# Optimization experiments

Measured on AMD Instinct MI355X. Metric: run time of the kernel, lower is better.

## Reference

```python
import jax, jax.numpy as jnp
import numpy as np

H = 8            # heads
M = 256          # num_landmarks
PINV_ITERS = 6
PAD = 16         # residual_conv_kernel(33)//2


def layernorm(x, g, b, eps=1e-5):
    mu = x.mean(-1, keepdims=True)
    var = ((x - mu) ** 2).mean(-1, keepdims=True)
    return (x - mu) * jax.lax.rsqrt(var + eps) * g + b


def moore_penrose_pinv(x, iters=PINV_ITERS):
    # iterative Moore-Penrose pseudo-inverse (Nystromformer)
    abs_x = jnp.abs(x)
    col = abs_x.sum(-1)
    row = abs_x.sum(-2)
    z = jnp.swapaxes(x, -1, -2) / (jnp.max(col) * jnp.max(row))
    eye = jnp.eye(x.shape[-1], dtype=x.dtype)
    for _ in range(iters):
        xz = x @ z
        z = 0.25 * z @ (13.0 * eye - xz @ (15.0 * eye - xz @ (7.0 * eye - xz)))
    return z


def attn_block(y, ln1_g, ln1_b, w_qkv, w_out, b_out, res_w,
               ln2_g, ln2_b, w1, b1, w2, b2):
    B, N, D = y.shape
    inner = w_qkv.shape[1] // 3
    dh = inner // H
    xn = layernorm(y, ln1_g, ln1_b)
    qkv = xn @ w_qkv                      # [B,N,3*inner]
    q, k, v = jnp.split(qkv, 3, axis=-1)
    to_heads = lambda t: t.reshape(B, N, H, dh).transpose(0, 2, 1, 3)  # [B,H,N,dh]
    q, k, v = map(to_heads, (q, k, v))
    q = q * (dh ** -0.5)
    l = N // M                            # tokens per landmark (N % M == 0 here)
    q_l = q.reshape(B, H, M, l, dh).mean(3)  # sum/l == mean -> [B,H,M,dh]
    k_l = k.reshape(B, H, M, l, dh).mean(3)
    attn1 = jax.nn.softmax(jnp.einsum('bhnd,bhmd->bhnm', q, k_l), axis=-1)
    attn2 = jax.nn.softmax(jnp.einsum('bhid,bhjd->bhij', q_l, k_l), axis=-1)
    attn3 = jax.nn.softmax(jnp.einsum('bhmd,bhnd->bhmn', q_l, k), axis=-1)
    attn2_inv = moore_penrose_pinv(attn2)
    out = (attn1 @ attn2_inv) @ (attn3 @ v)   # [B,H,N,dh]
    # depthwise residual conv over sequence dim: v as NCHW with C=H, Hdim=N, Wdim=dh
    res = jax.lax.conv_general_dilated(
        v, res_w, window_strides=(1, 1), padding=[(PAD, PAD), (0, 0)],
        dimension_numbers=('NCHW', 'OIHW', 'NCHW'), feature_group_count=H)
    out = out + res
    out = out.transpose(0, 2, 1, 3).reshape(B, N, inner)
    y = y + out @ w_out + b_out
    yn = layernorm(y, ln2_g, ln2_b)
    hdn = jax.nn.gelu(yn @ w1 + b1, approximate=False)
    return y + hdn @ w2 + b2


def setup_inputs() -> dict:
    key = jax.random.key(0)
    ks = jax.random.split(key, 8)
    B, N, D, NB = 4, 4096, 256, 2
    inner = D
    p = lambda k, shp: jax.random.normal(k, shp, jnp.float32) * 0.02
    return {
        'x': jax.random.normal(ks[0], (B, N, D), jnp.float32),
        'ln1_g': jnp.ones((NB, D), jnp.float32),
        'ln1_b': jnp.zeros((NB, D), jnp.float32),
        'w_qkv': p(ks[1], (NB, D, 3 * inner)),
        'w_out': p(ks[2], (NB, inner, D)),
        'b_out': jnp.zeros((NB, D), jnp.float32),
        'res_w': p(ks[3], (NB, H, 1, 33, 1)),
        'ln2_g': jnp.ones((NB, D), jnp.float32),
        'ln2_b': jnp.zeros((NB, D), jnp.float32),
        'w1': p(ks[4], (NB, D, 2 * D)),
        'b1': jnp.zeros((NB, 2 * D), jnp.float32),
        'w2': p(ks[5], (NB, 2 * D, D)),
        'b2': jnp.zeros((NB, D), jnp.float32),
    }


def reference(x, ln1_g, ln1_b, w_qkv, w_out, b_out, res_w,
              ln2_g, ln2_b, w1, b1, w2, b2):
    y = x
    for i in range(ln1_g.shape[0]):
        y = attn_block(y, ln1_g[i], ln1_b[i], w_qkv[i], w_out[i], b_out[i],
                       res_w[i], ln2_g[i], ln2_b[i], w1[i], b1[i], w2[i], b2[i])
    return y
```

## Files before the change

kernel.cpp:

```cpp
#include <hip/hip_runtime.h>
#include <math.h>

typedef float f32x4 __attribute__((ext_vector_type(4)));
typedef short s16x8 __attribute__((ext_vector_type(8)));
typedef unsigned short u16;
typedef unsigned int u32;

#define MFMA16(a,b,c) __builtin_amdgcn_mfma_f32_16x16x32_bf16((a),(b),(c),0,0,0)
#define AS1 __attribute__((address_space(1)))
#define AS3 __attribute__((address_space(3)))

__device__ __forceinline__ void dma16(const u16* g, u16* l){
  __builtin_amdgcn_global_load_lds((const AS1 u32*)g, (AS3 u32*)l, 16, 0, 0);
}

__device__ __forceinline__ float bf2f(u16 u){
  union { unsigned int i; float f; } v; v.i = ((unsigned int)u)<<16; return v.f;
}
__device__ __forceinline__ u16 f2bf(float f){
  union { float f; unsigned int i; } v; v.f = f;
  unsigned int x = v.i;
  return (u16)((x + 0x7fffu + ((x>>16)&1u))>>16);
}

enum { EPI_QKV=0, EPI_BIAS_GELU=3 };

template<int EPI>
__global__ __launch_bounds__(256)
void kgemm2(const u16* __restrict__ A, const u16* __restrict__ BT, int K, int lda, int ldb,
            const float* __restrict__ bias, u16* __restrict__ outb, int ldc,
            u16* __restrict__ qo, u16* __restrict__ ko, u16* __restrict__ vo,
            u16* __restrict__ qlm, u16* __restrict__ klm)
{
  __shared__ __align__(16) u16 As[128*32];
  __shared__ __align__(16) u16 Bs[128*32];
  const int tid = threadIdx.x;
  const int w = tid>>6, wy = w>>1, wx = w&1, l = tid&63, q = l>>4, ln = l&15;
  const int m0 = blockIdx.x*128, n0 = blockIdx.y*128;
  const int lrow = l>>2, lch = l&3;

  f32x4 acc[4][4];
  #pragma unroll
  for (int i=0;i<4;i++)
    #pragma unroll
    for (int j=0;j<4;j++){ acc[i][j][0]=0.f; acc[i][j][1]=0.f; acc[i][j][2]=0.f; acc[i][j][3]=0.f; }

  for (int k0=0; k0<K; k0+=32){
    #pragma unroll
    for (int c=0;c<2;c++){
      int row = 32*w + 16*c + lrow;
      int gch = lch ^ ((row>>1)&3);
      dma16(A + (long)(m0+row)*lda + k0 + gch*8, &As[(32*w+16*c)*32]);
      dma16(BT + (long)(n0+row)*ldb + k0 + gch*8, &Bs[(32*w+16*c)*32]);
    }
    __syncthreads();
    s16x8 af[4], bfr[4];
    #pragma unroll
    for (int mt=0;mt<4;mt++){
      int row = wy*64 + mt*16 + ln;
      af[mt] = *(const s16x8*)&As[row*32 + ((q ^ ((row>>1)&3))<<3)];
    }
    #pragma unroll
    for (int nt=0;nt<4;nt++){
      int row = wx*64 + nt*16 + ln;
      bfr[nt] = *(const s16x8*)&Bs[row*32 + ((q ^ ((row>>1)&3))<<3)];
    }
    #pragma unroll
    for (int mt=0;mt<4;mt++)
      #pragma unroll
      for (int nt=0;nt<4;nt++)
        acc[mt][nt] = MFMA16(af[mt], bfr[nt], acc[mt][nt]);
    __syncthreads();
  }

  #pragma unroll
  for (int mt=0;mt<4;mt++)
  #pragma unroll
  for (int nt=0;nt<4;nt++){
    int ncol = n0 + wx*64 + nt*16 + ln;
    if (EPI==EPI_QKV){
      int sel = ncol>>8, hd = ncol&255, h = hd>>5, d = hd&31;
      u16* dst = sel==0 ? qo : (sel==1 ? ko : vo);
      float sc2 = (sel==0) ? 0.17677669529663689f : 1.f;
      float s = 0.f;
      #pragma unroll
      for (int r=0;r<4;r++){
        int mrow = m0 + wy*64 + mt*16 + q*4 + r;
        int b = mrow>>12, n = mrow&4095;
        float v = acc[mt][nt][r]*sc2;
        dst[(((long)(b*8+h)*4096 + n)<<5) + d] = f2bf(v);
        s += v;
      }
      if (sel < 2){
        s += __shfl_xor(s, 16);
        s += __shfl_xor(s, 32);
        if (q == 0){
          int mrow0 = m0 + wy*64 + mt*16;
          int b = mrow0>>12, grp = (mrow0&4095)>>4;
          u16* ldst = (sel==0) ? qlm : klm;
          ldst[(((long)(b*8+h)*256 + grp)<<5) + d] = f2bf(s*(1.0f/16.0f));
        }
      }
    } else {
      #pragma unroll
      for (int r=0;r<4;r++){
        int mrow = m0 + wy*64 + mt*16 + q*4 + r;
        float x = acc[mt][nt][r] + bias[ncol];
        float g = 0.5f*x*(1.0f + erff(x*0.70710678118654752f));
        outb[(long)mrow*ldc + ncol] = f2bf(g);
      }
    }
  }
}

__global__ __launch_bounds__(256)
void kgemmLN(const u16* __restrict__ A, const u16* __restrict__ BT, int K,
             const float* __restrict__ bias, const float* __restrict__ base,
             float* __restrict__ yout,
             const float* __restrict__ lng, const float* __restrict__ lnb,
             u16* __restrict__ xnout)
{
  __shared__ __align__(16) u16 As[64*32];
  __shared__ __align__(16) u16 Bs[256*32];
  __shared__ float red[64][4];
  const int tid = threadIdx.x;
  const int w = tid>>6, l = tid&63, q = l>>4, ln = l&15;
  const int m0 = blockIdx.x*64;

  f32x4 acc[4][4];
  #pragma unroll
  for (int i=0;i<4;i++)
    #pragma unroll
    for (int j=0;j<4;j++){ acc[i][j][0]=0.f; acc[i][j][1]=0.f; acc[i][j][2]=0.f; acc[i][j][3]=0.f; }

  for (int k0=0; k0<K; k0+=32){
    {
      int row = w*16 + (l>>2);
      int gch = (l&3) ^ ((row>>1)&3);
      dma16(A + (long)(m0+row)*K + k0 + gch*8, &As[(w*16)*32]);
    }
    #pragma unroll
    for (int c=0;c<4;c++){
      int row = c*64 + w*16 + (l>>2);
      int gch = (l&3) ^ ((row>>1)&3);
      dma16(BT + (long)row*K + k0 + gch*8, &Bs[(c*64+w*16)*32]);
    }
    __syncthreads();
    s16x8 af[4], bfr[4];
    #pragma unroll
    for (int mt=0;mt<4;mt++){
      int row = mt*16 + ln;
      af[mt] = *(const s16x8*)&As[row*32 + ((q ^ ((row>>1)&3))<<3)];
    }
    #pragma unroll
    for (int nt=0;nt<4;nt++){
      int row = w*64 + nt*16 + ln;
      bfr[nt] = *(const s16x8*)&Bs[row*32 + ((q ^ ((row>>1)&3))<<3)];
    }
    #pragma unroll
    for (int mt=0;mt<4;mt++)
      #pragma unroll
      for (int nt=0;nt<4;nt++)
        acc[mt][nt] = MFMA16(af[mt], bfr[nt], acc[mt][nt]);
    __syncthreads();
  }

  float rb[4];
  #pragma unroll
  for (int nt=0;nt<4;nt++) rb[nt] = bias[w*64 + nt*16 + ln];
  #pragma unroll
  for (int mt=0;mt<4;mt++)
  #pragma unroll
  for (int r=0;r<4;r++){
    long rowb = (long)(m0 + mt*16 + q*4 + r)*256;
    #pragma unroll
    for (int nt=0;nt<4;nt++){
      int col = w*64 + nt*16 + ln;
      float v = base[rowb + col] + acc[mt][nt][r] + rb[nt];
      acc[mt][nt][r] = v;
      yout[rowb + col] = v;
    }
  }
  #pragma unroll
  for (int mt=0;mt<4;mt++)
  #pragma unroll
  for (int r=0;r<4;r++){
    float s = acc[mt][0][r]+acc[mt][1][r]+acc[mt][2][r]+acc[mt][3][r];
    s += __shfl_xor(s,1); s += __shfl_xor(s,2); s += __shfl_xor(s,4); s += __shfl_xor(s,8);
    if (ln==0) red[mt*16+q*4+r][w] = s;
  }
  __syncthreads();
  float mu[4][4];
  #pragma unroll
  for (int mt=0;mt<4;mt++)
  #pragma unroll
  for (int r=0;r<4;r++){
    int row = mt*16+q*4+r;
    mu[mt][r] = (red[row][0]+red[row][1]+red[row][2]+red[row][3])*(1.0f/256.0f);
  }
  __syncthreads();
  #pragma unroll
  for (int mt=0;mt<4;mt++)
  #pragma unroll
  for (int r=0;r<4;r++){
    float vs = 0.f;
    #pragma unroll
    for (int nt=0;nt<4;nt++){ float d = acc[mt][nt][r]-mu[mt][r]; vs += d*d; }
    vs += __shfl_xor(vs,1); vs += __shfl_xor(vs,2); vs += __shfl_xor(vs,4); vs += __shfl_xor(vs,8);
    if (ln==0) red[mt*16+q*4+r][w] = vs;
  }
  __syncthreads();
  float rg[4], rbb[4];
  #pragma unroll
  for (int nt=0;nt<4;nt++){ int col = w*64+nt*16+ln; rg[nt]=lng[col]; rbb[nt]=lnb[col]; }
  #pragma unroll
  for (int mt=0;mt<4;mt++)
  #pragma unroll
  for (int r=0;r<4;r++){
    int row = mt*16+q*4+r;
    float rs = rsqrtf((red[row][0]+red[row][1]+red[row][2]+red[row][3])*(1.0f/256.0f) + 1e-5f);
    long rowb = (long)(m0 + row)*256;
    #pragma unroll
    for (int nt=0;nt<4;nt++){
      int col = w*64 + nt*16 + ln;
      float d = acc[mt][nt][r]-mu[mt][r];
      xnout[rowb + col] = f2bf(d*rs*rg[nt] + rbb[nt]);
    }
  }
}

__device__ __forceinline__ int swidx(int row, int col){
  int cc = col>>3;
  int sl = (cc&24)|((cc&7)^((row>>1)&7));
  return row*256 + sl*8 + (col&7);
}
__device__ __forceinline__ int slot8(int ca, int row){
  return ((ca&24)|((ca&7)^((row>>1)&7)))<<3;
}

__device__ __forceinline__ void stage256(const u16* __restrict__ g, u16* lds, int w, int l){
  const int drow = l>>5, dch = l&31;
  #pragma unroll
  for (int c=0;c<16;c++){
    int base = (c*8 + w)*2;
    int row = base + drow;
    int gch = (dch&24) | ((dch&7) ^ ((row>>1)&7));
    dma16(g + (long)row*256 + gch*8, &lds[base*256]);
  }
}
__device__ __forceinline__ void stage32(const u16* __restrict__ g, u16* lds, int w, int l){
  const int drow = l>>5, dch = l&31;
  #pragma unroll
  for (int c=0;c<2;c++){
    int base = (c*8 + w)*2;
    int row = base + drow;
    int gch = (dch&24) | ((dch&7) ^ ((row>>1)&7));
    dma16(g + (long)row*256 + gch*8, &lds[base*256]);
  }
}
__device__ __forceinline__ void stage16(const u16* __restrict__ g, u16* lds, int w, int l){
  const int drow = l>>5, dch = l&31;
  int row = w*2 + drow;
  int gch = (dch&24) | ((dch&7) ^ ((row>>1)&7));
  dma16(g + (long)row*256 + gch*8, &lds[(w*2)*256]);
}

__device__ __forceinline__ void loadBf(const u16* bL, int w, int l, s16x8 (&bw)[2][8]){
  const int q=l>>4, ln=l&15, wn0=w*32;
  #pragma unroll
  for (int nt=0;nt<2;nt++)
    #pragma unroll
    for (int kq=0;kq<8;kq++){
      int n = wn0 + nt*16 + ln, ca = kq*4+q;
      bw[nt][kq] = *(const s16x8*)&bL[n*256 + slot8(ca, n)];
    }
}

__device__ __forceinline__ void multAr(const u16* aL, int arow0, const s16x8 (&bw)[2][8],
                                       int l, f32x4 (&acc)[2][2]){
  const int q=l>>4, ln=l&15;
  #pragma unroll
  for (int mt=0;mt<2;mt++)
    #pragma unroll
    for (int nt=0;nt<2;nt++){ acc[mt][nt][0]=0.f; acc[mt][nt][1]=0.f; acc[mt][nt][2]=0.f; acc[mt][nt][3]=0.f; }
  #pragma unroll
  for (int kq=0;kq<8;kq++){
    int ca = kq*4+q;
    s16x8 af[2];
    #pragma unroll
    for (int mt=0;mt<2;mt++){
      int r = arow0 + mt*16 + ln;
      af[mt] = *(const s16x8*)&aL[r*256 + slot8(ca, r)];
    }
    #pragma unroll
    for (int mt=0;mt<2;mt++)
      #pragma unroll
      for (int nt=0;nt<2;nt++)
        acc[mt][nt] = MFMA16(af[mt], bw[nt][kq], acc[mt][nt]);
  }
}

__device__ __forceinline__ void multHr(const u16* hL, const s16x8 (&bw)[2][8],
                                       int l, f32x4 (&hacc)[2]){
  const int q=l>>4, ln=l&15;
  hacc[0][0]=0.f; hacc[0][1]=0.f; hacc[0][2]=0.f; hacc[0][3]=0.f;
  hacc[1][0]=0.f; hacc[1][1]=0.f; hacc[1][2]=0.f; hacc[1][3]=0.f;
  #pragma unroll
  for (int kq=0;kq<8;kq++){
    int ca = kq*4+q;
    s16x8 af = *(const s16x8*)&hL[ln*256 + slot8(ca, ln)];
    hacc[0] = MFMA16(af, bw[0][kq], hacc[0]);
    hacc[1] = MFMA16(af, bw[1][kq], hacc[1]);
  }
}

__device__ __forceinline__ void polyinit13(const u16* aL, int arow0, int w, int l, f32x4 (&poly)[2][2]){
  const int q=l>>4, ln=l&15, wn0=w*32;
  #pragma unroll
  for (int mt=0;mt<2;mt++)
  #pragma unroll
  for (int nt=0;nt<2;nt++)
  #pragma unroll
  for (int r=0;r<4;r++){
    int row = arow0 + mt*16 + q*4 + r;
    int col = wn0 + nt*16 + ln;
    poly[mt][nt][r] = 13.f*bf2f(aL[swidx(row,col)]);
  }
}
__device__ __forceinline__ void init13H(const u16* hL, int w, int l, f32x4 (&hpoly)[2]){
  const int q=l>>4, ln=l&15, wn0=w*32;
  #pragma unroll
  for (int nt=0;nt<2;nt++)
  #pragma unroll
  for (int r=0;r<4;r++)
    hpoly[nt][r] = 13.f*bf2f(hL[swidx(q*4+r, wn0+nt*16+ln)]);
}
__device__ __forceinline__ void polyaxpy(f32x4 (&poly)[2][2], const f32x4 (&acc)[2][2], float sc){
  #pragma unroll
  for (int mt=0;mt<2;mt++)
    #pragma unroll
    for (int nt=0;nt<2;nt++)
      #pragma unroll
      for (int r=0;r<4;r++) poly[mt][nt][r] += sc*acc[mt][nt][r];
}
__device__ __forceinline__ void axpyH(f32x4 (&hpoly)[2], const f32x4 (&hacc)[2], float sc){
  #pragma unroll
  for (int nt=0;nt<2;nt++)
    #pragma unroll
    for (int r=0;r<4;r++) hpoly[nt][r] += sc*hacc[nt][r];
}
__device__ __forceinline__ void writeT(u16* Ts, const f32x4 (&acc)[2][2], int w, int l, float sc){
  const int q=l>>4, ln=l&15, wn0=w*32;
  #pragma unroll
  for (int mt=0;mt<2;mt++)
  #pragma unroll
  for (int nt=0;nt<2;nt++)
  #pragma unroll
  for (int r=0;r<4;r++){
    int row = mt*16 + q*4 + r;
    int col = wn0 + nt*16 + ln;
    Ts[swidx(row,col)] = f2bf(sc*acc[mt][nt][r]);
  }
}
__device__ __forceinline__ void writeH(u16* Hs, const f32x4 (&hacc)[2], int w, int l){
  const int q=l>>4, ln=l&15, wn0=w*32;
  #pragma unroll
  for (int nt=0;nt<2;nt++)
  #pragma unroll
  for (int r=0;r<4;r++)
    Hs[swidx(q*4+r, wn0+nt*16+ln)] = f2bf(hacc[nt][r]);
}
__device__ __forceinline__ void epi_poly(u16* __restrict__ out, int rowbase,
                                         const f32x4 (&poly)[2][2], int w, int l, float sc){
  const int q=l>>4, ln=l&15, wn0=w*32;
  #pragma unroll
  for (int mt=0;mt<2;mt++)
  #pragma unroll
  for (int nt=0;nt<2;nt++)
  #pragma unroll
  for (int r=0;r<4;r++){
    int row = rowbase + mt*16 + q*4 + r;
    int col = wn0 + nt*16 + ln;
    out[(long)row*256 + col] = f2bf(sc*poly[mt][nt][r]);
  }
}
__device__ __forceinline__ void epiH(u16* __restrict__ out, const f32x4 (&hpoly)[2],
                                     int w, int l, float sc){
  const int q=l>>4, ln=l&15, wn0=w*32;
  #pragma unroll
  for (int nt=0;nt<2;nt++)
  #pragma unroll
  for (int r=0;r<4;r++)
    out[(long)(q*4+r)*256 + wn0+nt*16+ln] = f2bf(sc*hpoly[nt][r]);
}

__device__ __forceinline__ void mult32(const u16* aL, int arow0, const u16* bL,
                                       int w, int l, f32x4 (&acc)[2][2]){
  const int q=l>>4, ln=l&15, wn0=w*32;
  #pragma unroll
  for (int mt=0;mt<2;mt++)
    #pragma unroll
    for (int nt=0;nt<2;nt++){ acc[mt][nt][0]=0.f; acc[mt][nt][1]=0.f; acc[mt][nt][2]=0.f; acc[mt][nt][3]=0.f; }
  #pragma unroll
  for (int kq=0;kq<8;kq++){
    int ca = kq*4+q;
    s16x8 af[2];
    #pragma unroll
    for (int mt=0;mt<2;mt++){
      int r = arow0 + mt*16 + ln;
      af[mt] = *(const s16x8*)&aL[r*256 + slot8(ca,r)];
    }
    #pragma unroll
    for (int nt=0;nt<2;nt++){
      int n = wn0 + nt*16 + ln;
      s16x8 bfr = *(const s16x8*)&bL[n*256 + slot8(ca,n)];
      acc[0][nt] = MFMA16(af[0], bfr, acc[0][nt]);
      acc[1][nt] = MFMA16(af[1], bfr, acc[1][nt]);
    }
  }
}

__global__ __launch_bounds__(512)
void kw0(const float* __restrict__ cs_p, float* __restrict__ scal,
         const float* __restrict__ num_p, const float* __restrict__ den_p,
         const u16* __restrict__ X, u16* __restrict__ W0, u16* __restrict__ h0)
{
  __shared__ __align__(16) u16 Wf[65536];
  __shared__ __align__(16) u16 Ts[8192];
  const int tid=threadIdx.x, w=tid>>6, l=tid&63;
  const int bid=blockIdx.x, xcd=bid&7, j=bid>>3;
  const int batch = xcd*4 + (j>>3), slab = j&7;

  stage256(X + (long)batch*65536, Wf, w, l);

  float* red = (float*)Ts;
  float mx = 0.f;
  for (int i=tid;i<8192;i+=512){
    float s = 0.f;
    #pragma unroll
    for (int c=0;c<8;c++) s += cs_p[(long)c*8192 + i];
    mx = fmaxf(mx, s);
  }
  red[tid] = mx; __syncthreads();
  for (int s=256;s>0;s>>=1){ if (tid<s) red[tid] = fmaxf(red[tid], red[tid+s]); __syncthreads(); }
  float s0 = 1.0f/red[0];
  if (bid==0 && tid==0) scal[0] = s0;

  f32x4 acc[2][2];
  mult32(Wf, slab*32, Wf, w, l, acc);
  {
    const int q=l>>4, ln=l&15, wn0=w*32;
    u16* ob = W0 + (long)batch*65536;
    #pragma unroll
    for (int mt=0;mt<2;mt++)
    #pragma unroll
    for (int nt=0;nt<2;nt++)
    #pragma unroll
    for (int r=0;r<4;r++){
      int row = slab*32 + mt*16 + q*4 + r;
      int col = wn0 + nt*16 + ln;
      ob[(long)row*256 + col] = f2bf(acc[mt][nt][r]*s0);
    }
  }

  if (slab==0){
    __syncthreads();
    float (*lt)[257] = (float(*)[257])Wf;
    for (int i=tid;i<8192;i+=512){
      int m = i>>5, d = i&31;
      float sn = 0.f, sd = 0.f;
      #pragma unroll
      for (int c=0;c<8;c++){
        sn += num_p[((long)(c*32+batch))*8192 + i];
        sd += den_p[(c*32+batch)*256 + m];
      }
      lt[d][m] = sn/sd;
    }
    __syncthreads();
    u16* o = h0 + (long)batch*8192;
    for (int j2=tid;j2<8192;j2+=512){
      int d = j2>>8, m = j2&255;
      o[j2] = f2bf(lt[d][m]);
    }
  }
}

__global__ __launch_bounds__(512)
void kiter(const u16* __restrict__ Win, u16* __restrict__ Wout,
           const u16* __restrict__ hin, u16* __restrict__ hout)
{
  __shared__ __align__(16) u16 Wf[65536];
  __shared__ __align__(16) u16 Ts[8192];
  __shared__ __align__(16) u16 Hs[4096];
  const int tid=threadIdx.x, w=tid>>6, l=tid&63;
  const int bid=blockIdx.x, xcd=bid&7, j=bid>>3;
  const int batch = xcd*4 + (j>>3), slab = j&7;
  const bool hrole = (slab&3)==0;
  const int hr0 = (slab>>2)*16;

  stage256(Win + (long)batch*65536, Wf, w, l);
  if (hrole) stage16(hin + (long)batch*8192 + hr0*256, Hs, w, l);
  __syncthreads();

  s16x8 bw[2][8];
  loadBf(Wf, w, l, bw);

  f32x4 acc[2][2], poly[2][2];
  f32x4 hacc[2], hpoly[2];

  polyinit13(Wf, slab*32, w, l, poly);
  multAr(Wf, slab*32, bw, l, acc);
  polyaxpy(poly, acc, -15.f);
  if (hrole){
    init13H(Hs, w, l, hpoly);
    multHr(Hs, bw, l, hacc);
    axpyH(hpoly, hacc, -15.f);
  }
  __syncthreads();
  writeT(Ts, acc, w, l, 1.f);
  if (hrole) writeH(Hs, hacc, w, l);
  __syncthreads();
  multAr(Ts, 0, bw, l, acc);
  polyaxpy(poly, acc, 7.f);
  if (hrole){ multHr(Hs, bw, l, hacc); axpyH(hpoly, hacc, 7.f); }
  __syncthreads();
  writeT(Ts, acc, w, l, 1.f);
  if (hrole) writeH(Hs, hacc, w, l);
  __syncthreads();
  multAr(Ts, 0, bw, l, acc);
  polyaxpy(poly, acc, -1.f);
  epi_poly(Wout + (long)batch*65536, slab*32, poly, w, l, 0.25f);
  if (hrole){
    multHr(Hs, bw, l, hacc);
    axpyH(hpoly, hacc, -1.f);
    epiH(hout + (long)batch*8192 + hr0*256, hpoly, w, l, 0.25f);
  }
}

__global__ __launch_bounds__(512)
void ktail(const u16* __restrict__ W5, const u16* __restrict__ h5,
           const u16* __restrict__ XT, const float* __restrict__ scal,
           u16* __restrict__ uT)
{
  __shared__ __align__(16) u16 Wf[65536];
  __shared__ __align__(16) u16 Ts[8192];
  const int tid=threadIdx.x, w=tid>>6, l=tid&63;
  const int batch = blockIdx.x;

  stage256(W5 + (long)batch*65536, Wf, w, l);
  stage32(h5 + (long)batch*8192, Ts, w, l);
  __syncthreads();

  s16x8 bw[2][8];
  loadBf(Wf, w, l, bw);

  f32x4 acc[2][2], poly[2][2];
  polyinit13(Ts, 0, w, l, poly);
  multAr(Ts, 0, bw, l, acc);
  polyaxpy(poly, acc, -15.f);
  __syncthreads(); writeT(Ts, acc, w, l, 1.f); __syncthreads();
  multAr(Ts, 0, bw, l, acc);
  polyaxpy(poly, acc, 7.f);
  __syncthreads(); writeT(Ts, acc, w, l, 1.f); __syncthreads();
  multAr(Ts, 0, bw, l, acc);
  polyaxpy(poly, acc, -1.f);
  __syncthreads();
  writeT(Ts, poly, w, l, 0.25f);
  stage256(XT + (long)batch*65536, Wf, w, l);
  __syncthreads();
  loadBf(Wf, w, l, bw);
  multAr(Ts, 0, bw, l, acc);
  const float s0 = scal[0];
  {
    const int q=l>>4, ln=l&15, wn0=w*32;
    u16* ob = uT + (long)batch*8192;
    #pragma unroll
    for (int mt=0;mt<2;mt++)
    #pragma unroll
    for (int nt=0;nt<2;nt++)
    #pragma unroll
    for (int r=0;r<4;r++){
      int row = mt*16 + q*4 + r;
      int col = wn0 + nt*16 + ln;
      ob[(long)row*256 + col] = f2bf(acc[mt][nt][r]*s0);
    }
  }
}

__global__ __launch_bounds__(256)
void kattn23(const u16* __restrict__ ql, const u16* __restrict__ kl,
             u16* __restrict__ X, u16* __restrict__ XT, float* __restrict__ cs_p,
             const u16* __restrict__ kk, const u16* __restrict__ vv,
             float* __restrict__ num_p, float* __restrict__ den_p)
{
  __shared__ __align__(16) u16 Pbuf[4][64][40];
  __shared__ __align__(16) u16 vT[32][40];
  __shared__ float qrow[32][33];
  __shared__ float psum[32][4];
  __shared__ float rsum[32];
  int bh = blockIdx.y;
  int tid = threadIdx.x, w = tid>>6, l = tid&63, q = l>>4, ln = l&15;

  if (blockIdx.x < 8){
    int r0 = blockIdx.x*32;
    int c = tid;
    #pragma unroll
    for (int i=0;i<4;i++){
      int e = c*4+i; int rr = e>>5, dd = e&31;
      qrow[rr][dd] = bf2f(ql[((long)bh*256 + r0+rr)*32 + dd]);
    }
    float kc[32];
    {
      const u16* kp = kl + ((long)bh*256 + c)*32;
      #pragma unroll
      for (int d=0;d<32;d++) kc[d] = bf2f(kp[d]);
    }
    __syncthreads();
    float er[32]; float colacc = 0.f;
    for (int r=0;r<32;r++){
      float s = 0.f;
      #pragma unroll
      for (int d=0;d<32;d++) s += qrow[r][d]*kc[d];
      float e = __expf(s);
      er[r] = e;
      float wsum = e;
      #pragma unroll
      for (int m=1;m<64;m<<=1) wsum += __shfl_xor(wsum, m);
      if (l==0) psum[r][w] = wsum;
    }
    __syncthreads();
    if (c<32) rsum[c] = psum[c][0]+psum[c][1]+psum[c][2]+psum[c][3];
    __syncthreads();
    for (int r=0;r<32;r++){
      float x = er[r]/rsum[r];
      u16 xb = f2bf(x);
      X [((long)bh*256 + r0+r)*256 + c] = xb;
      XT[((long)bh*256 + c)*256 + r0+r] = xb;
      colacc += x;
    }
    cs_p[(long)blockIdx.x*8192 + bh*256 + c] = colacc;
    return;
  }

  int chunk = blockIdx.x - 8;
  f32x4 z4; z4[0]=0.f; z4[1]=0.f; z4[2]=0.f; z4[3]=0.f;
  f32x4 acc[4][2]; f32x4 dacc[4];
  #pragma unroll
  for (int mt=0;mt<4;mt++){ dacc[mt]=z4; acc[mt][0]=z4; acc[mt][1]=z4; }
  const u16* qlb = ql + (long)bh*8192;
  const u16* kb  = kk + (long)bh*131072;
  const u16* vb  = vv + (long)bh*131072;
  int vn = tid>>3, vd = (tid&7)*4;
  for (int s=0;s<16;s++){
    int n0 = chunk*512 + s*32;
    ushort4 vx = *(const ushort4*)(vb + (long)(n0+vn)*32 + vd);
    vT[vd+0][vn]=vx.x; vT[vd+1][vn]=vx.y; vT[vd+2][vn]=vx.z; vT[vd+3][vn]=vx.w;
    __syncthreads();
    s16x8 bk[2];
    #pragma unroll
    for (int nt=0;nt<2;nt++) bk[nt] = *(const s16x8*)(kb + (long)(n0 + nt*16 + ln)*32 + q*8);
    #pragma unroll
    for (int mt=0;mt<4;mt++){
      s16x8 aq = *(const s16x8*)(qlb + (long)(w*64 + mt*16 + ln)*32 + q*8);
      #pragma unroll
      for (int nt=0;nt<2;nt++){
        f32x4 sf = MFMA16(aq, bk[nt], z4);
        f32x4 ef;
        #pragma unroll
        for (int r=0;r<4;r++) ef[r] = __expf(sf[r]);
        dacc[mt] += ef;
        #pragma unroll
        for (int r=0;r<4;r++) Pbuf[w][mt*16 + q*4 + r][nt*16 + ln] = f2bf(ef[r]);
      }
    }
    #pragma unroll
    for (int mt=0;mt<4;mt++){
      s16x8 ap = *(const s16x8*)&Pbuf[w][mt*16 + ln][q*8];
      #pragma unroll
      for (int nt=0;nt<2;nt++){
        s16x8 bv = *(const s16x8*)&vT[nt*16 + ln][q*8];
        acc[mt][nt] = MFMA16(ap, bv, acc[mt][nt]);
      }
    }
    __syncthreads();
  }
  #pragma unroll
  for (int mt=0;mt<4;mt++)
    #pragma unroll
    for (int r=0;r<4;r++){
      float x = dacc[mt][r];
      x += __shfl_xor(x,1); x += __shfl_xor(x,2); x += __shfl_xor(x,4); x += __shfl_xor(x,8);
      dacc[mt][r] = x;
    }
  long pbase = (long)(chunk*32 + bh);
  #pragma unroll
  for (int mt=0;mt<4;mt++)
    #pragma unroll
    for (int nt=0;nt<2;nt++)
      #pragma unroll
      for (int r=0;r<4;r++){
        int mg = w*64 + mt*16 + q*4 + r;
        num_p[pbase*8192 + (long)mg*32 + nt*16 + ln] = acc[mt][nt][r];
      }
  if (ln==0){
    #pragma unroll
    for (int mt=0;mt<4;mt++)
      #pragma unroll
      for (int r=0;r<4;r++)
        den_p[pbase*256 + w*64 + mt*16 + q*4 + r] = dacc[mt][r];
  }
}

__global__ __launch_bounds__(256)
void kattn1u(const u16* __restrict__ qq, const u16* __restrict__ kl, const u16* __restrict__ uT,
             const u16* __restrict__ vv, const float* __restrict__ rw,
             u16* __restrict__ aoutb)
{
  int nch = blockIdx.x, bh = blockIdx.y;
  int b = bh>>3, h = bh&7;
  int tid = threadIdx.x, w = tid>>6, l = tid&63, q = l>>4, ln = l&15;
  __shared__ __align__(16) u16 Pbuf[4][32][40];
  __shared__ __align__(16) u16 vtile[160][36];
  int r0g = nch*128;
  const u16* vb = vv + (long)bh*131072;
  #pragma unroll
  for (int it=0; it<5; it++){
    int slot = tid + it*256;
    int rr = slot>>3, c = (slot&7)*4;
    int s = r0g - 16 + rr;
    ushort4 val; val.x=0; val.y=0; val.z=0; val.w=0;
    if (s>=0 && s<4096) val = *(const ushort4*)(vb + (long)s*32 + c);
    *(ushort4*)&vtile[rr][c] = val;
  }
  __syncthreads();

  f32x4 z4; z4[0]=0.f; z4[1]=0.f; z4[2]=0.f; z4[3]=0.f;
  f32x4 acc[2][2]; f32x4 dacc[2];
  #pragma unroll
  for (int mt=0;mt<2;mt++){ dacc[mt]=z4; acc[mt][0]=z4; acc[mt][1]=z4; }
  const u16* qb  = qq + (long)bh*131072;
  const u16* klb = kl + (long)bh*8192;
  const u16* ub  = uT + (long)bh*8192;
  int r0 = r0g + w*32;
  for (int s=0;s<8;s++){
    s16x8 bk[2];
    #pragma unroll
    for (int nt=0;nt<2;nt++) bk[nt] = *(const s16x8*)(klb + (long)(s*32 + nt*16 + ln)*32 + q*8);
    #pragma unroll
    for (int mt=0;mt<2;mt++){
      s16x8 aq = *(const s16x8*)(qb + (long)(r0 + mt*16 + ln)*32 + q*8);
      #pragma unroll
      for (int nt=0;nt<2;nt++){
        f32x4 sf = MFMA16(aq, bk[nt], z4);
        f32x4 ef;
        #pragma unroll
        for (int r=0;r<4;r++) ef[r] = __expf(sf[r]);
        dacc[mt] += ef;
        #pragma unroll
        for (int r=0;r<4;r++) Pbuf[w][mt*16 + q*4 + r][nt*16 + ln] = f2bf(ef[r]);
      }
    }
    #pragma unroll
    for (int mt=0;mt<2;mt++){
      s16x8 ap = *(const s16x8*)&Pbuf[w][mt*16 + ln][q*8];
      #pragma unroll
      for (int nt=0;nt<2;nt++){
        s16x8 bu = *(const s16x8*)(ub + (long)(nt*16 + ln)*256 + s*32 + q*8);
        acc[mt][nt] = MFMA16(ap, bu, acc[mt][nt]);
      }
    }
  }
  #pragma unroll
  for (int mt=0;mt<2;mt++)
    #pragma unroll
    for (int r=0;r<4;r++){
      float x = dacc[mt][r];
      x += __shfl_xor(x,1); x += __shfl_xor(x,2); x += __shfl_xor(x,4); x += __shfl_xor(x,8);
      dacc[mt][r] = x;
    }

  const float* wp = rw + h*33;
  float w_[33];
  #pragma unroll
  for (int j=0;j<33;j++) w_[j] = wp[j];

  #pragma unroll
  for (int mt=0;mt<2;mt++){
    int nl = w*32 + mt*16 + q*4;
    #pragma unroll
    for (int nt=0;nt<2;nt++){
      int d = nt*16 + ln;
      float vvv[36];
      #pragma unroll
      for (int j=0;j<36;j++) vvv[j] = bf2f(vtile[nl + j][d]);
      #pragma unroll
      for (int r=0;r<4;r++){
        float cv = 0.f;
        #pragma unroll
        for (int j=0;j<33;j++) cv += w_[j]*vvv[r+j];
        int n = r0 + mt*16 + q*4 + r;
        long oidx = ((long)b*4096 + n)*256 + h*32 + d;
        aoutb[oidx] = f2bf(acc[mt][nt][r]/dacc[mt][r] + cv);
      }
    }
  }
}

__global__ __launch_bounds__(256)
void kcvtln(const float* __restrict__ xin, const float* __restrict__ lg, const float* __restrict__ lb,
            u16* __restrict__ xn,
            const float* __restrict__ wqkv, const float* __restrict__ wout,
            const float* __restrict__ w1, const float* __restrict__ w2,
            u16* __restrict__ wqkvT, u16* __restrict__ woutT,
            u16* __restrict__ w1T, u16* __restrict__ w2T)
{
  __shared__ float t[32][33];
  int z = blockIdx.x;
  if (z < 4096){
    int w = threadIdx.x>>6, l = threadIdx.x&63;
    long row = (long)z*4 + w;
    float4 v = ((const float4*)(xin + row*256))[l];
    float s = v.x+v.y+v.z+v.w;
    #pragma unroll
    for (int m=1;m<64;m<<=1) s += __shfl_xor(s, m);
    float mu = s*(1.0f/256.0f);
    float dx=v.x-mu, dy=v.y-mu, dz=v.z-mu, dw=v.w-mu;
    float s2 = dx*dx+dy*dy+dz*dz+dw*dw;
    #pragma unroll
    for (int m=1;m<64;m<<=1) s2 += __shfl_xor(s2, m);
    float rs = rsqrtf(s2*(1.0f/256.0f) + 1e-5f);
    float4 gg = ((const float4*)lg)[l];
    float4 bb = ((const float4*)lb)[l];
    ushort4 o;
    o.x = f2bf(dx*rs*gg.x + bb.x);
    o.y = f2bf(dy*rs*gg.y + bb.y);
    o.z = f2bf(dz*rs*gg.z + bb.z);
    o.w = f2bf(dw*rs*gg.w + bb.w);
    *(ushort4*)(xn + row*256 + l*4) = o;
    return;
  }
  z -= 4096;
  const float* src; u16* dst; int K, Nn, bx, by;
  if (z < 384){      int i=z/192, r=z%192; src=wqkv+(long)i*196608; dst=wqkvT+(long)i*196608; K=256; Nn=768; bx=r%24; by=r/24; }
  else if (z < 512){ int zz=z-384; int i=zz/64, r=zz%64; src=wout+(long)i*65536; dst=woutT+(long)i*65536; K=256; Nn=256; bx=r%8; by=r/8; }
  else if (z < 768){ int zz=z-512; int i=zz/128, r=zz%128; src=w1+(long)i*131072; dst=w1T+(long)i*131072; K=256; Nn=512; bx=r%16; by=r/16; }
  else {             int zz=z-768; int i=zz/128, r=zz%128; src=w2+(long)i*131072; dst=w2T+(long)i*131072; K=512; Nn=256; bx=r%8; by=r/8; }
  int n0 = bx*32, k0 = by*32;
  int tx = threadIdx.x&31, ty = threadIdx.x>>5;
  #pragma unroll
  for (int i=0;i<4;i++) t[ty+i*8][tx] = src[(long)(k0+ty+i*8)*Nn + n0+tx];
  __syncthreads();
  #pragma unroll
  for (int i=0;i<4;i++) dst[(long)(n0+ty+i*8)*K + k0+tx] = f2bf(t[tx][ty+i*8]);
}

extern "C" void kernel_launch(void* const* d_in, const int* in_sizes, int n_in,
                              void* d_out, int out_size, void* d_ws, size_t ws_size,
                              hipStream_t stream)
{
  const float* x    = (const float*)d_in[0];
  const float* ln1g = (const float*)d_in[1];
  const float* ln1b = (const float*)d_in[2];
  const float* wqkv = (const float*)d_in[3];
  const float* wout = (const float*)d_in[4];
  const float* bout = (const float*)d_in[5];
  const float* resw = (const float*)d_in[6];
  const float* ln2g = (const float*)d_in[7];
  const float* ln2b = (const float*)d_in[8];
  const float* w1   = (const float*)d_in[9];
  const float* b1   = (const float*)d_in[10];
  const float* w2   = (const float*)d_in[11];
  const float* b2   = (const float*)d_in[12];
  float* y = (float*)d_out;
  char* ws = (char*)d_ws;

  u16* xn    = (u16*)(ws + 0);
  u16* qb    = (u16*)(ws + 8388608);
  u16* kb    = (u16*)(ws + 16777216);
  u16* vb    = (u16*)(ws + 25165824);
  u16* ql    = (u16*)(ws + 33554432);
  u16* kl    = (u16*)(ws + 34078720);
  u16* X     = (u16*)(ws + 34603008);
  u16* XT    = (u16*)(ws + 38797312);
  u16* h0b   = (u16*)(ws + 42991616);
  u16* WA    = (u16*)(ws + 51380224);
  u16* WB    = (u16*)(ws + 55574528);
  u16* hA    = (u16*)(ws + 68157440);
  u16* hB    = (u16*)(ws + 72351744);
  float* num_p = (float*)(ws + 76546048);
  float* den_p = (float*)(ws + 84934656);
  float* cs_p  = (float*)(ws + 85196800);
  float* scal  = (float*)(ws + 85458944);
  u16* uT    = (u16*)(ws + 85459200);
  u16* aoutb = (u16*)(ws + 85983488);
  u16* wqkvT = (u16*)(ws + 94372096);
  u16* woutT = (u16*)(ws + 95158528);
  u16* w1T   = (u16*)(ws + 95420672);
  u16* w2T   = (u16*)(ws + 95944960);
  u16* hdn   = (u16*)(ws + 51380224);

  (void)in_sizes; (void)n_in; (void)out_size; (void)ws_size;

  kcvtln<<<5120,256,0,stream>>>(x, ln1g, ln1b, xn,
      wqkv, wout, w1, w2, wqkvT, woutT, w1T, w2T);

  for (int i=0;i<2;i++){
    kgemm2<EPI_QKV><<<dim3(128,6),256,0,stream>>>(xn, wqkvT + (long)i*196608, 256, 256, 256,
        nullptr, nullptr, 0, qb,kb,vb, ql,kl);
    kattn23<<<dim3(16,32),256,0,stream>>>(ql, kl, X, XT, cs_p, kb, vb, num_p, den_p);

    kw0<<<256,512,0,stream>>>(cs_p, scal, num_p, den_p, X, WA, h0b);
    u16 *Wi = WA, *Wo = WB, *hi = h0b, *ho = hA;
    for (int it=0; it<5; it++){
      kiter<<<256,512,0,stream>>>(Wi, Wo, hi, ho);
      u16* t = Wi; Wi = Wo; Wo = t;
      hi = ho; ho = (ho == hA) ? hB : hA;
    }
    ktail<<<32,512,0,stream>>>(Wi, hi, XT, scal, uT);

    kattn1u<<<dim3(32,32),256,0,stream>>>(qb, kl, uT, vb, resw + i*264, aoutb);
    kgemmLN<<<256,256,0,stream>>>(aoutb, woutT + (long)i*65536, 256,
        bout + i*256, i==0 ? x : y, y, ln2g + i*256, ln2b + i*256, xn);
    kgemm2<EPI_BIAS_GELU><<<dim3(128,4),256,0,stream>>>(xn, w1T + (long)i*131072, 256, 256, 256,
        b1 + i*512, hdn, 512, nullptr,nullptr,nullptr, nullptr,nullptr);
    kgemmLN<<<256,256,0,stream>>>(hdn, w2T + (long)i*131072, 512,
        b2 + i*256, y, y, ln1g + 256, ln1b + 256, xn);
  }
}
```

Measured before the change: 501.6 us.

## Double-buffer V tile, hoist Q fragments, transpose conv V tile for vector reads

In kattn23, the V tile is now double-buffered in shared memory. The next tile is loaded from global memory while the current one is being consumed, which removes one barrier per iteration. Q-landmark fragments are hoisted out of the loop in both attention kernels. In kattn1u, the residual-conv V tile is stored transposed so each thread reads 36 consecutive values with 9 ushort4 loads instead of 36 scalar strided loads. These changes add shared memory and register pressure, and the transposed scalar LDS stores may cause bank conflicts.

After: 621.0 us. 23.8% more time.

```diff
diff --git a/kernel.cpp b/kernel.cpp
--- a/kernel.cpp
+++ b/kernel.cpp
@@ -594,7 +594,7 @@
              float* __restrict__ num_p, float* __restrict__ den_p)
 {
   __shared__ __align__(16) u16 Pbuf[4][64][40];
-  __shared__ __align__(16) u16 vT[32][40];
+  __shared__ __align__(16) u16 vT2[2][32][40];
   __shared__ float qrow[32][33];
   __shared__ float psum[32][4];
   __shared__ float rsum[32];
@@ -650,21 +650,28 @@
   const u16* qlb = ql + (long)bh*8192;
   const u16* kb  = kk + (long)bh*131072;
   const u16* vb  = vv + (long)bh*131072;
+  s16x8 aq[4];
+  #pragma unroll
+  for (int mt=0;mt<4;mt++) aq[mt] = *(const s16x8*)(qlb + (long)(w*64 + mt*16 + ln)*32 + q*8);
   int vn = tid>>3, vd = (tid&7)*4;
+  {
+    ushort4 vx = *(const ushort4*)(vb + (long)(chunk*512+vn)*32 + vd);
+    vT2[0][vd+0][vn]=vx.x; vT2[0][vd+1][vn]=vx.y; vT2[0][vd+2][vn]=vx.z; vT2[0][vd+3][vn]=vx.w;
+  }
+  __syncthreads();
   for (int s=0;s<16;s++){
+    int cur = s&1;
+    ushort4 vnx;
+    if (s<15) vnx = *(const ushort4*)(vb + (long)(chunk*512+(s+1)*32+vn)*32 + vd);
     int n0 = chunk*512 + s*32;
-    ushort4 vx = *(const ushort4*)(vb + (long)(n0+vn)*32 + vd);
-    vT[vd+0][vn]=vx.x; vT[vd+1][vn]=vx.y; vT[vd+2][vn]=vx.z; vT[vd+3][vn]=vx.w;
-    __syncthreads();
     s16x8 bk[2];
     #pragma unroll
     for (int nt=0;nt<2;nt++) bk[nt] = *(const s16x8*)(kb + (long)(n0 + nt*16 + ln)*32 + q*8);
     #pragma unroll
     for (int mt=0;mt<4;mt++){
-      s16x8 aq = *(const s16x8*)(qlb + (long)(w*64 + mt*16 + ln)*32 + q*8);
       #pragma unroll
       for (int nt=0;nt<2;nt++){
-        f32x4 sf = MFMA16(aq, bk[nt], z4);
+        f32x4 sf = MFMA16(aq[mt], bk[nt], z4);
         f32x4 ef;
         #pragma unroll
         for (int r=0;r<4;r++) ef[r] = __expf(sf[r]);
@@ -678,9 +685,13 @@
       s16x8 ap = *(const s16x8*)&Pbuf[w][mt*16 + ln][q*8];
       #pragma unroll
       for (int nt=0;nt<2;nt++){
-        s16x8 bv = *(const s16x8*)&vT[nt*16 + ln][q*8];
+        s16x8 bv = *(const s16x8*)&vT2[cur][nt*16 + ln][q*8];
         acc[mt][nt] = MFMA16(ap, bv, acc[mt][nt]);
       }
+    }
+    if (s<15){
+      int nxt = cur^1;
+      vT2[nxt][vd+0][vn]=vnx.x; vT2[nxt][vd+1][vn]=vnx.y; vT2[nxt][vd+2][vn]=vnx.z; vT2[nxt][vd+3][vn]=vnx.w;
     }
     __syncthreads();
   }
@@ -720,7 +731,7 @@
   int b = bh>>3, h = bh&7;
   int tid = threadIdx.x, w = tid>>6, l = tid&63, q = l>>4, ln = l&15;
   __shared__ __align__(16) u16 Pbuf[4][32][40];
-  __shared__ __align__(16) u16 vtile[160][36];
+  __shared__ __align__(16) u16 vtileT[32][164];
   int r0g = nch*128;
   const u16* vb = vv + (long)bh*131072;
   #pragma unroll
@@ -730,7 +741,7 @@
     int s = r0g - 16 + rr;
     ushort4 val; val.x=0; val.y=0; val.z=0; val.w=0;
     if (s>=0 && s<4096) val = *(const ushort4*)(vb + (long)s*32 + c);
-    *(ushort4*)&vtile[rr][c] = val;
+    vtileT[c+0][rr]=val.x; vtileT[c+1][rr]=val.y; vtileT[c+2][rr]=val.z; vtileT[c+3][rr]=val.w;
   }
   __syncthreads();
 
@@ -742,16 +753,18 @@
   const u16* klb = kl + (long)bh*8192;
   const u16* ub  = uT + (long)bh*8192;
   int r0 = r0g + w*32;
+  s16x8 aq[2];
+  #pragma unroll
+  for (int mt=0;mt<2;mt++) aq[mt] = *(const s16x8*)(qb + (long)(r0 + mt*16 + ln)*32 + q*8);
   for (int s=0;s<8;s++){
     s16x8 bk[2];
     #pragma unroll
     for (int nt=0;nt<2;nt++) bk[nt] = *(const s16x8*)(klb + (long)(s*32 + nt*16 + ln)*32 + q*8);
     #pragma unroll
     for (int mt=0;mt<2;mt++){
-      s16x8 aq = *(const s16x8*)(qb + (long)(r0 + mt*16 + ln)*32 + q*8);
       #pragma unroll
       for (int nt=0;nt<2;nt++){
-        f32x4 sf = MFMA16(aq, bk[nt], z4);
+        f32x4 sf = MFMA16(aq[mt], bk[nt], z4);
         f32x4 ef;
         #pragma unroll
         for (int r=0;r<4;r++) ef[r] = __expf(sf[r]);
@@ -791,8 +804,13 @@
     for (int nt=0;nt<2;nt++){
       int d = nt*16 + ln;
       float vvv[36];
-      #pragma unroll
-      for (int j=0;j<36;j++) vvv[j] = bf2f(vtile[nl + j][d]);
+      const u16* vp = &vtileT[d][nl];
+      #pragma unroll
+      for (int jj=0;jj<9;jj++){
+        ushort4 vq = *(const ushort4*)(vp + jj*4);
+        vvv[jj*4+0]=bf2f(vq.x); vvv[jj*4+1]=bf2f(vq.y);
+        vvv[jj*4+2]=bf2f(vq.z); vvv[jj*4+3]=bf2f(vq.w);
+      }
       #pragma unroll
       for (int r=0;r<4;r++){
         float cv = 0.f;
```

## Replace final pinv iteration with row-slab polynomial chain in split tail kernel

Applied to the files above, without the earlier changes.

Drops one full 256x256 Newton-Schulz iteration launch. In its place the new tail kernel applies the remaining polynomial steps only to the 32-row h slab, blending them through a fixed linear combination (gpoly) before multiplying by XT. The tail work is split over two blocks per batch, and the XT staging is overlapped with the polynomial chain. This removes a large matrix-matrix pass in exchange for a long serial chain of small row-slab products with many barriers, and its numerical equivalence to the original iteration is not obvious.

Result: no change. 493.3 us (-1.7%).

```diff
diff --git a/kernel.cpp b/kernel.cpp
--- a/kernel.cpp
+++ b/kernel.cpp
@@ -248,16 +248,6 @@
     dma16(g + (long)row*256 + gch*8, &lds[base*256]);
   }
 }
-__device__ __forceinline__ void stage32(const u16* __restrict__ g, u16* lds, int w, int l){
-  const int drow = l>>5, dch = l&31;
-  #pragma unroll
-  for (int c=0;c<2;c++){
-    int base = (c*8 + w)*2;
-    int row = base + drow;
-    int gch = (dch&24) | ((dch&7) ^ ((row>>1)&7));
-    dma16(g + (long)row*256 + gch*8, &lds[base*256]);
-  }
-}
 __device__ __forceinline__ void stage16(const u16* __restrict__ g, u16* lds, int w, int l){
   const int drow = l>>5, dch = l&31;
   int row = w*2 + drow;
@@ -349,6 +339,10 @@
     #pragma unroll
     for (int r=0;r<4;r++) hpoly[nt][r] += sc*hacc[nt][r];
 }
+__device__ __forceinline__ void zeroH(f32x4 (&p)[2]){
+  p[0][0]=0.f; p[0][1]=0.f; p[0][2]=0.f; p[0][3]=0.f;
+  p[1][0]=0.f; p[1][1]=0.f; p[1][2]=0.f; p[1][3]=0.f;
+}
 __device__ __forceinline__ void writeT(u16* Ts, const f32x4 (&acc)[2][2], int w, int l, float sc){
   const int q=l>>4, ln=l&15, wn0=w*32;
   #pragma unroll
@@ -369,6 +363,14 @@
   #pragma unroll
   for (int r=0;r<4;r++)
     Hs[swidx(q*4+r, wn0+nt*16+ln)] = f2bf(hacc[nt][r]);
+}
+__device__ __forceinline__ void writeHsc(u16* Hs, const f32x4 (&v)[2], int w, int l, float sc){
+  const int q=l>>4, ln=l&15, wn0=w*32;
+  #pragma unroll
+  for (int nt=0;nt<2;nt++)
+  #pragma unroll
+  for (int r=0;r<4;r++)
+    Hs[swidx(q*4+r, wn0+nt*16+ln)] = f2bf(sc*v[nt][r]);
 }
 __device__ __forceinline__ void epi_poly(u16* __restrict__ out, int rowbase,
                                          const f32x4 (&poly)[2][2], int w, int l, float sc){
@@ -538,53 +540,69 @@
 }
 
 __global__ __launch_bounds__(512)
-void ktail(const u16* __restrict__ W5, const u16* __restrict__ h5,
-           const u16* __restrict__ XT, const float* __restrict__ scal,
-           u16* __restrict__ uT)
+void ktail2(const u16* __restrict__ W4, const u16* __restrict__ h4,
+            const u16* __restrict__ XT, const float* __restrict__ scal,
+            u16* __restrict__ uT)
 {
   __shared__ __align__(16) u16 Wf[65536];
-  __shared__ __align__(16) u16 Ts[8192];
+  __shared__ __align__(16) u16 Ha[4096];
+  __shared__ __align__(16) u16 Hb[4096];
   const int tid=threadIdx.x, w=tid>>6, l=tid&63;
-  const int batch = blockIdx.x;
-
-  stage256(W5 + (long)batch*65536, Wf, w, l);
-  stage32(h5 + (long)batch*8192, Ts, w, l);
+  const int batch = blockIdx.x>>1, half = blockIdx.x&1;
+
+  stage256(W4 + (long)batch*65536, Wf, w, l);
+  stage16(h4 + (long)batch*8192 + half*4096, Ha, w, l);
   __syncthreads();
 
   s16x8 bw[2][8];
   loadBf(Wf, w, l, bw);
-
-  f32x4 acc[2][2], poly[2][2];
-  polyinit13(Ts, 0, w, l, poly);
-  multAr(Ts, 0, bw, l, acc);
-  polyaxpy(poly, acc, -15.f);
-  __syncthreads(); writeT(Ts, acc, w, l, 1.f); __syncthreads();
-  multAr(Ts, 0, bw, l, acc);
-  polyaxpy(poly, acc, 7.f);
-  __syncthreads(); writeT(Ts, acc, w, l, 1.f); __syncthreads();
-  multAr(Ts, 0, bw, l, acc);
-  polyaxpy(poly, acc, -1.f);
-  __syncthreads();
-  writeT(Ts, poly, w, l, 0.25f);
+  __syncthreads();
   stage256(XT + (long)batch*65536, Wf, w, l);
-  __syncthreads();
+
+  f32x4 acc[2], poly[2], gpoly[2];
+
+  init13H(Ha, w, l, poly);
+  multHr(Ha, bw, l, acc); axpyH(poly, acc, -15.f);
+  writeH(Hb, acc, w, l); __syncthreads();
+  multHr(Hb, bw, l, acc); axpyH(poly, acc, 7.f);
+  writeH(Ha, acc, w, l); __syncthreads();
+  multHr(Ha, bw, l, acc); axpyH(poly, acc, -1.f);
+  zeroH(gpoly); axpyH(gpoly, poly, 3.25f);
+  writeHsc(Hb, poly, w, l, 0.25f); __syncthreads();
+
+  multHr(Hb, bw, l, acc); zeroH(poly); axpyH(poly, acc, 13.f);
+  writeH(Ha, acc, w, l); __syncthreads();
+  multHr(Ha, bw, l, acc); axpyH(poly, acc, -15.f);
+  writeH(Hb, acc, w, l); __syncthreads();
+  multHr(Hb, bw, l, acc); axpyH(poly, acc, 7.f);
+  writeH(Ha, acc, w, l); __syncthreads();
+  multHr(Ha, bw, l, acc); axpyH(poly, acc, -1.f);
+  axpyH(gpoly, poly, -3.75f);
+  writeHsc(Hb, poly, w, l, 0.25f); __syncthreads();
+
+  multHr(Hb, bw, l, acc); zeroH(poly); axpyH(poly, acc, 13.f);
+  writeH(Ha, acc, w, l); __syncthreads();
+  multHr(Ha, bw, l, acc); axpyH(poly, acc, -15.f);
+  writeH(Hb, acc, w, l); __syncthreads();
+  multHr(Hb, bw, l, acc); axpyH(poly, acc, 7.f);
+  writeH(Ha, acc, w, l); __syncthreads();
+  multHr(Ha, bw, l, acc); axpyH(poly, acc, -1.f);
+  axpyH(gpoly, poly, 1.75f);
+  writeHsc(Hb, poly, w, l, 0.25f); __syncthreads();
+
+  multHr(Hb, bw, l, acc); zeroH(poly); axpyH(poly, acc, 13.f);
+  writeH(Ha, acc, w, l); __syncthreads();
+  multHr(Ha, bw, l, acc); axpyH(poly, acc, -15.f);
+  writeH(Hb, acc, w, l); __syncthreads();
+  multHr(Hb, bw, l, acc); axpyH(poly, acc, 7.f);
+  writeH(Ha, acc, w, l); __syncthreads();
+  multHr(Ha, bw, l, acc); axpyH(poly, acc, -1.f);
+  axpyH(gpoly, poly, -0.25f);
+  writeHsc(Hb, gpoly, w, l, 0.25f); __syncthreads();
+
   loadBf(Wf, w, l, bw);
-  multAr(Ts, 0, bw, l, acc);
-  const float s0 = scal[0];
-  {
-    const int q=l>>4, ln=l&15, wn0=w*32;
-    u16* ob = uT + (long)batch*8192;
-    #pragma unroll
-    for (int mt=0;mt<2;mt++)
-    #pragma unroll
-    for (int nt=0;nt<2;nt++)
-    #pragma unroll
-    for (int r=0;r<4;r++){
-      int row = mt*16 + q*4 + r;
-      int col = wn0 + nt*16 + ln;
-      ob[(long)row*256 + col] = f2bf(acc[mt][nt][r]*s0);
-    }
-  }
+  multHr(Hb, bw, l, acc);
+  epiH(uT + (long)batch*8192 + half*4096, acc, w, l, scal[0]);
 }
 
 __global__ __launch_bounds__(256)
@@ -911,12 +929,12 @@
 
     kw0<<<256,512,0,stream>>>(cs_p, scal, num_p, den_p, X, WA, h0b);
     u16 *Wi = WA, *Wo = WB, *hi = h0b, *ho = hA;
-    for (int it=0; it<5; it++){
+    for (int it=0; it<4; it++){
       kiter<<<256,512,0,stream>>>(Wi, Wo, hi, ho);
       u16* t = Wi; Wi = Wo; Wo = t;
       hi = ho; ho = (ho == hA) ? hB : hA;
     }
-    ktail<<<32,512,0,stream>>>(Wi, hi, XT, scal, uT);
+    ktail2<<<64,512,0,stream>>>(Wi, hi, XT, scal, uT);
 
     kattn1u<<<dim3(32,32),256,0,stream>>>(qb, kl, uT, vb, resw + i*264, aoutb);
     kgemmLN<<<256,256,0,stream>>>(aoutb, woutT + (long)i*65536, 256,
```
